# Optimization experiments

Measured on AMD Instinct MI355X. Metric: run time of the kernel, lower is better.

The kernel has to match this reference:

```python
import jax, jax.numpy as jnp
import numpy as np

POI, EMB, UNITS, QDIM, B = 5000, 256, 512, 256, 64


def setup_inputs() -> dict:
    key = jax.random.key(0)
    ks = jax.random.split(key, 16)
    s = 0.05
    return {
        "x": jax.random.randint(ks[0], (B,), 0, POI),
        "query": jax.random.normal(ks[1], (B, QDIM), jnp.float32),
        "poi_embedding": jax.random.normal(ks[2], (POI, EMB), jnp.float32),
        "A_hat": jax.random.normal(ks[3], (B, B), jnp.float32),
        "dec_hidden": jax.random.normal(ks[4], (B, UNITS), jnp.float32),
        "cat_dec_hidden": jax.random.normal(ks[5], (1, B, UNITS), jnp.float32),
        # GRUCell params (keras order z, r, h; reset_after=True -> bias [2, 3*units])
        "gru_kernel": jax.random.normal(ks[6], (EMB + QDIM, 3 * UNITS), jnp.float32) * s,
        "gru_rec_kernel": jax.random.normal(ks[7], (UNITS, 3 * UNITS), jnp.float32) * s,
        "gru_bias": jax.random.normal(ks[8], (2, 3 * UNITS), jnp.float32) * s,
        # Bahdanau attention params
        "W1_w": jax.random.normal(ks[9], (EMB, UNITS), jnp.float32) * s,
        "W1_b": jnp.zeros((UNITS,), jnp.float32),
        "W2_w": jax.random.normal(ks[10], (UNITS, UNITS), jnp.float32) * s,
        "W2_b": jnp.zeros((UNITS,), jnp.float32),
        "V_w": jax.random.normal(ks[11], (UNITS, 1), jnp.float32) * s,
        "V_b": jnp.zeros((1,), jnp.float32),
        # output dense: concat(context EMB, output_ UNITS, cat_hidden UNITS) -> POI
        "fc_w": jax.random.normal(ks[12], (EMB + 2 * UNITS, POI), jnp.float32) * s,
        "fc_b": jnp.zeros((POI,), jnp.float32),
    }


def _gru_cell(x, h, kernel, rec_kernel, bias):
    # keras GRUCell, reset_after=True, gate order (z, r, h)
    xm = x @ kernel + bias[0]        # [B, 3U]
    hm = h @ rec_kernel + bias[1]    # [B, 3U]
    xz, xr, xh = jnp.split(xm, 3, axis=-1)
    hz, hr, hh = jnp.split(hm, 3, axis=-1)
    z = jax.nn.sigmoid(xz + hz)
    r = jax.nn.sigmoid(xr + hr)
    h_cand = jnp.tanh(xh + r * hh)
    h_new = z * h + (1.0 - z) * h_cand
    return h_new, h_new


def reference(x, query, poi_embedding, A_hat, dec_hidden, cat_dec_hidden,
              gru_kernel, gru_rec_kernel, gru_bias,
              W1_w, W1_b, W2_w, W2_b, V_w, V_b, fc_w, fc_b):
    emb = poi_embedding
    x1 = jnp.concatenate([emb[x], query], axis=1)          # [B, EMB+QDIM]
    output_, state = _gru_cell(x1, dec_hidden, gru_kernel, gru_rec_kernel, gru_bias)
    # Bahdanau attention: values are the full embedding table [POI, EMB]
    v_proj = emb @ W1_w + W1_b                              # [POI, U]
    q_proj = output_ @ W2_w + W2_b                          # [B, U]
    score = jnp.tanh(v_proj[None, :, :] + q_proj[:, None, :]) @ V_w + V_b  # [B, POI, 1]
    attn = jax.nn.softmax(score, axis=1)                    # [B, POI, 1]
    context = jnp.sum(attn * emb[None, :, :], axis=1)       # [B, EMB]
    out_cat = jnp.concatenate([context, output_, cat_dec_hidden[0]], axis=1)
    logits = out_cat @ fc_w + fc_b                          # [B, POI]
    return (logits, state, output_)
```

## Files before the change

kernel.cpp:

```cpp
#include <hip/hip_runtime.h>
#include <hip/hip_bf16.h>

typedef __bf16 bf16;
typedef __bf16 bf16x8 __attribute__((ext_vector_type(8)));
typedef float f32x4 __attribute__((ext_vector_type(4)));

#define BB 64
#define EMB 256
#define UNITS 512
#define POI 5000
#define KCAT 1280
#define SCLD 5024
#define NSPL 8
#define L2E 1.4426950408889634f

__device__ __forceinline__ float rcp_(float x){ return __builtin_amdgcn_rcpf(x); }
__device__ __forceinline__ float exp2_(float x){ return __builtin_amdgcn_exp2f(x); }

__device__ __forceinline__ f32x4 mm16f(const float* __restrict__ A, const float* __restrict__ B,
                                       int lda, int ldb, int K, int mr, int nc, int lane){
  int q = lane >> 4;
  f32x4 acc = {0.f,0.f,0.f,0.f};
  const float* ap = A + (size_t)mr*lda + q*8;
  const float* bp = B + (size_t)(q*8)*ldb + nc;
#pragma unroll 2
  for(int k0 = 0; k0 < K; k0 += 32){
    f32x4 a0 = *(const f32x4*)ap;
    f32x4 a1 = *(const f32x4*)(ap+4);
    bf16x8 a, b;
#pragma unroll
    for(int j=0;j<4;j++){ a[j] = (bf16)a0[j]; a[4+j] = (bf16)a1[j]; }
#pragma unroll
    for(int j=0;j<8;j++) b[j] = (bf16)bp[(size_t)j*ldb];
    acc = __builtin_amdgcn_mfma_f32_16x16x32_bf16(a, b, acc, 0, 0, 0);
    ap += 32; bp += (size_t)32*ldb;
  }
  return acc;
}

__global__ __launch_bounds__(256) void k_gru(const int* __restrict__ x,
    const float* __restrict__ query, const float* __restrict__ emb, const float* __restrict__ h0,
    const float* __restrict__ gruK, const float* __restrict__ gruR,
    float* __restrict__ xmP, float* __restrict__ hmP){
  int lane = threadIdx.x & 63, w = threadIdx.x >> 6;
  int col = blockIdx.x*16 + (lane & 15);
  int m = w*16 + (lane & 15);
  int z = blockIdx.z;
  const float* A; const float* B; int lda, mr;
  if(blockIdx.y == 0){
    B = gruK + (size_t)(z*256)*1536;
    if(z == 0){ A = emb;   mr = x[m]; lda = EMB; }
    else      { A = query; mr = m;    lda = 256; }
  } else {
    B = gruR + (size_t)(z*256)*1536;
    A = h0 + z*256; mr = m; lda = UNITS;
  }
  f32x4 acc = mm16f(A, B, lda, 1536, 256, mr, col, lane);
  float* C = (blockIdx.y ? hmP : xmP) + (size_t)z*BB*1536;
  int rb = w*16 + (lane >> 4)*4;
#pragma unroll
  for(int r=0;r<4;r++) C[(size_t)(rb+r)*1536 + col] = acc[r];
}

__global__ void k_gates(const float* __restrict__ xmP, const float* __restrict__ hmP,
                        const float* __restrict__ bias, const float* __restrict__ h0,
                        const float* __restrict__ catd,
                        float* __restrict__ hn, float* __restrict__ outc, float* __restrict__ dout){
  int b = blockIdx.x, u = threadIdx.x;
  for(int p=u;p<POI;p+=512) dout[(size_t)b*POI + p] = 0.f;
  const float* x0 = xmP + b*1536; const float* x1s = xmP + (size_t)BB*1536 + b*1536;
  const float* h0s = hmP + b*1536; const float* h1s = hmP + (size_t)BB*1536 + b*1536;
  float xz = x0[u]      + x1s[u]      + bias[u];
  float xg = x0[512+u]  + x1s[512+u]  + bias[512+u];
  float xh = x0[1024+u] + x1s[1024+u] + bias[1024+u];
  float hz = h0s[u]      + h1s[u]      + bias[1536+u];
  float hg = h0s[512+u]  + h1s[512+u]  + bias[2048+u];
  float hh = h0s[1024+u] + h1s[1024+u] + bias[2560+u];
  float z = rcp_(1.f + exp2_(-L2E*(xz+hz)));
  float r = rcp_(1.f + exp2_(-L2E*(xg+hg)));
  float ca = xh + r*hh;
  ca = fminf(fmaxf(ca, -15.f), 15.f);
  float e = exp2_(2.f*L2E*ca);
  float hc = (e - 1.f)*rcp_(e + 1.f);
  float h = h0[b*512+u];
  float v = z*h + (1.f - z)*hc;
  hn[b*512+u] = v;
  outc[b*KCAT + 256 + u] = v;
  outc[b*KCAT + 768 + u] = catd[(size_t)b*512 + u];
  dout[(size_t)POI*BB + (size_t)b*512 + u] = v;
  dout[(size_t)POI*BB + (size_t)BB*512 + (size_t)b*512 + u] = v;
}

__global__ __launch_bounds__(64) void k_qproj(const float* __restrict__ hn, const float* __restrict__ W2,
                        const float* __restrict__ W2b, float* __restrict__ Eq){
  int lane = threadIdx.x;
  int m0 = (blockIdx.x & 3)*16;
  int col = (blockIdx.x >> 2)*16 + (lane & 15);
  f32x4 acc = mm16f(hn, W2, UNITS, UNITS, UNITS, m0 + (lane & 15), col, lane);
  float bn = W2b[col];
  int rb = m0 + (lane >> 4)*4;
#pragma unroll
  for(int r=0;r<4;r++){
    float v = (acc[r] + bn)*(2.f*L2E);
    Eq[(rb+r)*UNITS + col] = exp2_(fminf(fmaxf(v, -28.f), 28.f));
  }
}

__global__ __launch_bounds__(256) void k_vscore(const float* __restrict__ emb, const float* __restrict__ W1,
    const float* __restrict__ W1b, const float* __restrict__ Eq,
    const float* __restrict__ Vw, float* __restrict__ scS){
  __shared__ float evs[16][68];
  __shared__ float Qs[64][68];
  __shared__ float vws[64];
  int t = threadIdx.x, lane = t & 63, w = t >> 6;
  int p0 = blockIdx.x*16, uh = blockIdx.y*64;
  int mr = p0 + (lane & 15); if(mr > POI-1) mr = POI-1;
  {
    int ncl = w*16 + (lane & 15);
    f32x4 acc = mm16f(emb, W1, EMB, UNITS, EMB, mr, uh + ncl, lane);
    float bn = W1b[uh + ncl];
    int rb = (lane >> 4)*4;
#pragma unroll
    for(int r=0;r<4;r++){
      float v = (acc[r] + bn)*(2.f*L2E);
      evs[rb+r][ncl] = exp2_(fminf(fmaxf(v, -28.f), 28.f));
    }
  }
  for(int i=t;i<4096;i+=256){ int b=i>>6, u=i&63; Qs[b][u] = Eq[b*UNITS + uh + u]; }
  if(t < 64) vws[t] = Vw[uh + t];
  __syncthreads();
  int tp = t & 7, tb = t >> 3;
  float s00=0.f, s01=0.f, s10=0.f, s11=0.f;
#pragma unroll
  for(int u4=0;u4<16;u4++){
    f32x4 e0 = *(f32x4*)&evs[2*tp][u4*4];
    f32x4 e1 = *(f32x4*)&evs[2*tp+1][u4*4];
    f32x4 q0 = *(f32x4*)&Qs[2*tb][u4*4];
    f32x4 q1 = *(f32x4*)&Qs[2*tb+1][u4*4];
    f32x4 w4 = *(f32x4*)&vws[u4*4];
#pragma unroll
    for(int e=0;e<4;e++){
      float wv = w4[e];
      s00 += wv * rcp_(e0[e]*q0[e] + 1.f);
      s01 += wv * rcp_(e0[e]*q1[e] + 1.f);
      s10 += wv * rcp_(e1[e]*q0[e] + 1.f);
      s11 += wv * rcp_(e1[e]*q1[e] + 1.f);
    }
  }
  float* s = scS + (size_t)blockIdx.y*BB*SCLD;
  int pA = p0 + 2*tp, bA = 2*tb;
  if(pA < POI)  { s[(size_t)bA*SCLD + pA]   = s00; s[(size_t)(bA+1)*SCLD + pA]   = s01; }
  if(pA+1 < POI){ s[(size_t)bA*SCLD + pA+1] = s10; s[(size_t)(bA+1)*SCLD + pA+1] = s11; }
}

__global__ __launch_bounds__(1024) void k_softmax(float* __restrict__ sc, float* __restrict__ outc){
  __shared__ float red[1024];
  int b = blockIdx.x, t = threadIdx.x;
  if(t < 256) outc[b*KCAT + t] = 0.f;
  float* sA = sc + (size_t)b*SCLD;
  float sum = 0.f;
  for(int p=t;p<POI;p+=1024){
    float a = sA[p];
#pragma unroll
    for(int y=1;y<NSPL;y++) a += sA[(size_t)y*BB*SCLD + p];
    float wv = exp2_(-2.f*L2E*a);
    sA[p] = wv;
    sum += wv;
  }
  red[t] = sum; __syncthreads();
  for(int o=512;o>0;o>>=1){ if(t<o) red[t]+=red[t+o]; __syncthreads(); }
  float iv = rcp_(red[0]);
  for(int p=t;p<POI;p+=1024) sA[p] *= iv;
  if(t < SCLD-POI) sA[POI + t] = 0.f;
}

__global__ __launch_bounds__(256) void k_ctx(const float* __restrict__ wb, const float* __restrict__ emb,
                                             float* __restrict__ outc){
  int lane = threadIdx.x & 63, w = threadIdx.x >> 6;
  int n = blockIdx.x*16 + (lane & 15);
  int ky = blockIdx.y;
  int kbeg = ky*384;
  int mr = w*16 + (lane & 15);
  f32x4 acc = mm16f(wb + kbeg, emb + (size_t)kbeg*EMB, SCLD, EMB, 384, mr, n, lane);
  if(ky == 12){
    int q = lane >> 4;
    const float* ap = wb + (size_t)mr*SCLD + 4992 + q*8;
    bf16x8 a, bfr;
#pragma unroll
    for(int j=0;j<8;j++) a[j] = (bf16)ap[j];
#pragma unroll
    for(int j=0;j<8;j++){
      int k = 4992 + q*8 + j; int kc = k < POI ? k : POI-1;
      bfr[j] = (bf16)emb[(size_t)kc*EMB + n];
    }
    acc = __builtin_amdgcn_mfma_f32_16x16x32_bf16(a, bfr, acc, 0, 0, 0);
  }
  int rb = w*16 + (lane >> 4)*4;
#pragma unroll
  for(int r=0;r<4;r++) atomicAdd(&outc[(size_t)(rb+r)*KCAT + n], acc[r]);
}

__global__ __launch_bounds__(256) void k_logits(const float* __restrict__ A, const float* __restrict__ Bw,
                        const float* __restrict__ fcb, float* __restrict__ out){
  int lane = threadIdx.x & 63, w = threadIdx.x >> 6;
  int n = blockIdx.x*16 + (lane & 15);
  int nc = n < POI ? n : POI-1;
  int ky = blockIdx.y, kbeg = ky*320;
  f32x4 acc = mm16f(A + kbeg, Bw + (size_t)kbeg*POI, KCAT, POI, 320,
                    w*16 + (lane & 15), nc, lane);
  int rb = w*16 + (lane >> 4)*4;
  if(n < POI){
    float bn = (ky == 0) ? fcb[n] : 0.f;
#pragma unroll
    for(int r=0;r<4;r++) atomicAdd(&out[(size_t)(rb+r)*POI + n], acc[r] + bn);
  }
}

extern "C" void kernel_launch(void* const* d_in, const int* in_sizes, int n_in,
                              void* d_out, int out_size, void* d_ws, size_t ws_size,
                              hipStream_t stream){
  const int*   x     = (const int*)d_in[0];
  const float* query = (const float*)d_in[1];
  const float* emb   = (const float*)d_in[2];
  const float* h0    = (const float*)d_in[4];
  const float* catd  = (const float*)d_in[5];
  const float* gruK  = (const float*)d_in[6];
  const float* gruR  = (const float*)d_in[7];
  const float* gruB  = (const float*)d_in[8];
  const float* W1    = (const float*)d_in[9];
  const float* W1b   = (const float*)d_in[10];
  const float* W2    = (const float*)d_in[11];
  const float* W2b   = (const float*)d_in[12];
  const float* Vw    = (const float*)d_in[13];
  const float* fcw   = (const float*)d_in[15];
  const float* fcb   = (const float*)d_in[16];
  float* out = (float*)d_out;

  char* ws = (char*)d_ws;
  size_t off = 0;
  auto alloc = [&](size_t bytes)->void*{ void* p = ws + off; off += (bytes + 255) & ~(size_t)255; return p; };
  float* outc = (float*)alloc((size_t)BB*KCAT*4);
  float* xmP  = (float*)alloc((size_t)2*BB*1536*4);
  float* hmP  = (float*)alloc((size_t)2*BB*1536*4);
  float* hn   = (float*)alloc((size_t)BB*512*4);
  float* Eq   = (float*)alloc((size_t)BB*512*4);
  float* sc   = (float*)alloc((size_t)NSPL*BB*SCLD*4);

  k_gru    <<<dim3(96,2,2), 256, 0, stream>>>(x, query, emb, h0, gruK, gruR, xmP, hmP);
  k_gates  <<<BB, 512, 0, stream>>>(xmP, hmP, gruB, h0, catd, hn, outc, out);
  k_qproj  <<<128, 64, 0, stream>>>(hn, W2, W2b, Eq);
  k_vscore <<<dim3(313,NSPL), 256, 0, stream>>>(emb, W1, W1b, Eq, Vw, sc);
  k_softmax<<<BB, 1024, 0, stream>>>(sc, outc);
  k_ctx    <<<dim3(16,13), 256, 0, stream>>>(sc, emb, outc);
  k_logits <<<dim3(313,4), 256, 0, stream>>>(outc, fcw, fcb, out);
}
```

Baseline: 238.2 us.

## Pre-transpose weights to bf16 K-major and replace logits atomics with split-K reduction

Adds a transpose kernel that converts fc_w, GRU kernels, W1, W2 and the embedding table into transposed bf16 copies each call, so every MFMA B-operand becomes one contiguous 16-byte load instead of eight strided float loads. The logits GEMM now writes two split-K partial buffers that a new reduction kernel sums with the bias, replacing the atomicAdd path and the zero-fill of the output. The vscore split drops from 8 to 4 with each block covering 128 units. The transpose pass rereads about 26 MB of weights on every call, which could cost more than the faster GEMM loads save.

```diff
diff --git a/kernel.cpp b/kernel.cpp
--- a/kernel.cpp
+++ b/kernel.cpp
@@ -2,6 +2,7 @@
 #include <hip/hip_bf16.h>
 
 typedef __bf16 bf16;
+typedef __bf16 bf16x4 __attribute__((ext_vector_type(4)));
 typedef __bf16 bf16x8 __attribute__((ext_vector_type(8)));
 typedef float f32x4 __attribute__((ext_vector_type(4)));
 
@@ -11,51 +12,93 @@
 #define POI 5000
 #define KCAT 1280
 #define SCLD 5024
-#define NSPL 8
+#define LGLD 5008
 #define L2E 1.4426950408889634f
 
 __device__ __forceinline__ float rcp_(float x){ return __builtin_amdgcn_rcpf(x); }
 __device__ __forceinline__ float exp2_(float x){ return __builtin_amdgcn_exp2f(x); }
 
-__device__ __forceinline__ f32x4 mm16f(const float* __restrict__ A, const float* __restrict__ B,
-                                       int lda, int ldb, int K, int mr, int nc, int lane){
+__device__ __forceinline__ f32x4 mm16bt(const float* __restrict__ A, const bf16* __restrict__ Bt,
+                                        int lda, int ldbk, int K, int mr, int nc,
+                                        int ka, int kb, int lane){
   int q = lane >> 4;
   f32x4 acc = {0.f,0.f,0.f,0.f};
-  const float* ap = A + (size_t)mr*lda + q*8;
-  const float* bp = B + (size_t)(q*8)*ldb + nc;
+  const float* ap = A + (size_t)mr*lda + ka + q*8;
+  const bf16* bp = Bt + (size_t)nc*ldbk + kb + q*8;
 #pragma unroll 2
   for(int k0 = 0; k0 < K; k0 += 32){
     f32x4 a0 = *(const f32x4*)ap;
     f32x4 a1 = *(const f32x4*)(ap+4);
-    bf16x8 a, b;
+    bf16x8 a;
 #pragma unroll
     for(int j=0;j<4;j++){ a[j] = (bf16)a0[j]; a[4+j] = (bf16)a1[j]; }
-#pragma unroll
-    for(int j=0;j<8;j++) b[j] = (bf16)bp[(size_t)j*ldb];
+    bf16x8 b = *(const bf16x8*)bp;
     acc = __builtin_amdgcn_mfma_f32_16x16x32_bf16(a, b, acc, 0, 0, 0);
-    ap += 32; bp += (size_t)32*ldb;
+    ap += 32; bp += 32;
   }
   return acc;
+}
+
+__global__ __launch_bounds__(256) void k_tr(const float* __restrict__ fcw, const float* __restrict__ gruK,
+    const float* __restrict__ gruR, const float* __restrict__ W1, const float* __restrict__ W2,
+    const float* __restrict__ emb, bf16* __restrict__ fcwT, bf16* __restrict__ gKT,
+    bf16* __restrict__ gRT, bf16* __restrict__ W1T, bf16* __restrict__ W2T, bf16* __restrict__ embT){
+  __shared__ float ls[64][65];
+  int bid = blockIdx.x, t = threadIdx.x;
+  const float* src; bf16* dst; int Ks, Ns, lddst, dRows, tn, tk;
+  if(bid < 1580){      src=fcw;  Ks=1280; Ns=5000; dst=fcwT; lddst=1280; dRows=5008; tn=bid/20; tk=bid%20; }
+  else if(bid < 1772){ int b=bid-1580; src=gruK; Ks=512; Ns=1536; dst=gKT; lddst=512; dRows=1536; tn=b/8; tk=b%8; }
+  else if(bid < 1964){ int b=bid-1772; src=gruR; Ks=512; Ns=1536; dst=gRT; lddst=512; dRows=1536; tn=b/8; tk=b%8; }
+  else if(bid < 1996){ int b=bid-1964; src=W1;   Ks=256; Ns=512;  dst=W1T; lddst=256; dRows=512;  tn=b/4; tk=b%4; }
+  else if(bid < 2060){ int b=bid-1996; src=W2;   Ks=512; Ns=512;  dst=W2T; lddst=512; dRows=512;  tn=b/8; tk=b%8; }
+  else {               int b=bid-2060; src=emb;  Ks=5000; Ns=256; dst=embT; lddst=5056; dRows=256; tn=b/79; tk=b%79; }
+  int n0 = tn*64, k0 = tk*64;
+  bool fullN = (n0 + 64 <= Ns);
+#pragma unroll
+  for(int ps=0; ps<4; ps++){
+    int r = (t>>4) + ps*16;
+    int sr = k0 + r; if(sr > Ks-1) sr = Ks-1;
+    int c4 = (t&15)*4;
+    if(fullN){
+      f32x4 v = *(const f32x4*)&src[(size_t)sr*Ns + n0 + c4];
+      ls[r][c4]=v[0]; ls[r][c4+1]=v[1]; ls[r][c4+2]=v[2]; ls[r][c4+3]=v[3];
+    } else {
+#pragma unroll
+      for(int i=0;i<4;i++){ int sc2 = n0+c4+i; if(sc2 > Ns-1) sc2 = Ns-1; ls[r][c4+i] = src[(size_t)sr*Ns + sc2]; }
+    }
+  }
+  __syncthreads();
+#pragma unroll
+  for(int ps=0; ps<4; ps++){
+    int rr = (t>>4) + ps*16;
+    int dr = n0 + rr;
+    if(dr < dRows){
+      int cc = (t&15)*4;
+      bf16x4 o;
+#pragma unroll
+      for(int i=0;i<4;i++) o[i] = (bf16)ls[cc+i][rr];
+      *(bf16x4*)&dst[(size_t)dr*lddst + k0 + cc] = o;
+    }
+  }
 }
 
 __global__ __launch_bounds__(256) void k_gru(const int* __restrict__ x,
     const float* __restrict__ query, const float* __restrict__ emb, const float* __restrict__ h0,
-    const float* __restrict__ gruK, const float* __restrict__ gruR,
+    const bf16* __restrict__ gKT, const bf16* __restrict__ gRT,
     float* __restrict__ xmP, float* __restrict__ hmP){
   int lane = threadIdx.x & 63, w = threadIdx.x >> 6;
   int col = blockIdx.x*16 + (lane & 15);
   int m = w*16 + (lane & 15);
   int z = blockIdx.z;
-  const float* A; const float* B; int lda, mr;
+  const float* A; const bf16* Bt; int lda, mr, ka;
   if(blockIdx.y == 0){
-    B = gruK + (size_t)(z*256)*1536;
-    if(z == 0){ A = emb;   mr = x[m]; lda = EMB; }
-    else      { A = query; mr = m;    lda = 256; }
+    Bt = gKT;
+    if(z == 0){ A = emb;   mr = x[m]; lda = EMB; ka = 0; }
+    else      { A = query; mr = m;    lda = 256; ka = 0; }
   } else {
-    B = gruR + (size_t)(z*256)*1536;
-    A = h0 + z*256; mr = m; lda = UNITS;
-  }
-  f32x4 acc = mm16f(A, B, lda, 1536, 256, mr, col, lane);
+    Bt = gRT; A = h0; mr = m; lda = UNITS; ka = z*256;
+  }
+  f32x4 acc = mm16bt(A, Bt, lda, 512, 256, mr, col, ka, z*256, lane);
   float* C = (blockIdx.y ? hmP : xmP) + (size_t)z*BB*1536;
   int rb = w*16 + (lane >> 4)*4;
 #pragma unroll
@@ -67,7 +110,6 @@
                         const float* __restrict__ catd,
                         float* __restrict__ hn, float* __restrict__ outc, float* __restrict__ dout){
   int b = blockIdx.x, u = threadIdx.x;
-  for(int p=u;p<POI;p+=512) dout[(size_t)b*POI + p] = 0.f;
   const float* x0 = xmP + b*1536; const float* x1s = xmP + (size_t)BB*1536 + b*1536;
   const float* h0s = hmP + b*1536; const float* h1s = hmP + (size_t)BB*1536 + b*1536;
   float xz = x0[u]      + x1s[u]      + bias[u];
@@ -91,12 +133,12 @@
   dout[(size_t)POI*BB + (size_t)BB*512 + (size_t)b*512 + u] = v;
 }
 
-__global__ __launch_bounds__(64) void k_qproj(const float* __restrict__ hn, const float* __restrict__ W2,
+__global__ __launch_bounds__(64) void k_qproj(const float* __restrict__ hn, const bf16* __restrict__ W2T,
                         const float* __restrict__ W2b, float* __restrict__ Eq){
   int lane = threadIdx.x;
   int m0 = (blockIdx.x & 3)*16;
   int col = (blockIdx.x >> 2)*16 + (lane & 15);
-  f32x4 acc = mm16f(hn, W2, UNITS, UNITS, UNITS, m0 + (lane & 15), col, lane);
+  f32x4 acc = mm16bt(hn, W2T, UNITS, UNITS, UNITS, m0 + (lane & 15), col, 0, 0, lane);
   float bn = W2b[col];
   int rb = m0 + (lane >> 4)*4;
 #pragma unroll
@@ -106,18 +148,19 @@
   }
 }
 
-__global__ __launch_bounds__(256) void k_vscore(const float* __restrict__ emb, const float* __restrict__ W1,
+__global__ __launch_bounds__(256) void k_vscore(const float* __restrict__ emb, const bf16* __restrict__ W1T,
     const float* __restrict__ W1b, const float* __restrict__ Eq,
     const float* __restrict__ Vw, float* __restrict__ scS){
-  __shared__ float evs[16][68];
+  __shared__ float evs[16][132];
   __shared__ float Qs[64][68];
-  __shared__ float vws[64];
+  __shared__ float vws[128];
   int t = threadIdx.x, lane = t & 63, w = t >> 6;
-  int p0 = blockIdx.x*16, uh = blockIdx.y*64;
+  int p0 = blockIdx.x*16, uh = blockIdx.y*128;
   int mr = p0 + (lane & 15); if(mr > POI-1) mr = POI-1;
-  {
-    int ncl = w*16 + (lane & 15);
-    f32x4 acc = mm16f(emb, W1, EMB, UNITS, EMB, mr, uh + ncl, lane);
+#pragma unroll
+  for(int i=0;i<2;i++){
+    int ncl = (w + i*4)*16 + (lane & 15);
+    f32x4 acc = mm16bt(emb, W1T, EMB, EMB, EMB, mr, uh + ncl, 0, 0, lane);
     float bn = W1b[uh + ncl];
     int rb = (lane >> 4)*4;
 #pragma unroll
@@ -126,25 +169,29 @@
       evs[rb+r][ncl] = exp2_(fminf(fmaxf(v, -28.f), 28.f));
     }
   }
-  for(int i=t;i<4096;i+=256){ int b=i>>6, u=i&63; Qs[b][u] = Eq[b*UNITS + uh + u]; }
-  if(t < 64) vws[t] = Vw[uh + t];
-  __syncthreads();
+  if(t < 128) vws[t] = Vw[uh + t];
   int tp = t & 7, tb = t >> 3;
   float s00=0.f, s01=0.f, s10=0.f, s11=0.f;
-#pragma unroll
-  for(int u4=0;u4<16;u4++){
-    f32x4 e0 = *(f32x4*)&evs[2*tp][u4*4];
-    f32x4 e1 = *(f32x4*)&evs[2*tp+1][u4*4];
-    f32x4 q0 = *(f32x4*)&Qs[2*tb][u4*4];
-    f32x4 q1 = *(f32x4*)&Qs[2*tb+1][u4*4];
-    f32x4 w4 = *(f32x4*)&vws[u4*4];
-#pragma unroll
-    for(int e=0;e<4;e++){
-      float wv = w4[e];
-      s00 += wv * rcp_(e0[e]*q0[e] + 1.f);
-      s01 += wv * rcp_(e0[e]*q1[e] + 1.f);
-      s10 += wv * rcp_(e1[e]*q0[e] + 1.f);
-      s11 += wv * rcp_(e1[e]*q1[e] + 1.f);
+  for(int c=0;c<2;c++){
+    __syncthreads();
+    int ub = c*64;
+    for(int i=t;i<4096;i+=256){ int b=i>>6, u=i&63; Qs[b][u] = Eq[b*UNITS + uh + ub + u]; }
+    __syncthreads();
+#pragma unroll
+    for(int u4=0;u4<16;u4++){
+      f32x4 e0 = *(f32x4*)&evs[2*tp][ub+u4*4];
+      f32x4 e1 = *(f32x4*)&evs[2*tp+1][ub+u4*4];
+      f32x4 q0 = *(f32x4*)&Qs[2*tb][u4*4];
+      f32x4 q1 = *(f32x4*)&Qs[2*tb+1][u4*4];
+      f32x4 w4 = *(f32x4*)&vws[ub+u4*4];
+#pragma unroll
+      for(int e=0;e<4;e++){
+        float wv = w4[e];
+        s00 += wv * rcp_(e0[e]*q0[e] + 1.f);
+        s01 += wv * rcp_(e0[e]*q1[e] + 1.f);
+        s10 += wv * rcp_(e1[e]*q0[e] + 1.f);
+        s11 += wv * rcp_(e1[e]*q1[e] + 1.f);
+      }
     }
   }
   float* s = scS + (size_t)blockIdx.y*BB*SCLD;
@@ -160,9 +207,7 @@
   float* sA = sc + (size_t)b*SCLD;
   float sum = 0.f;
   for(int p=t;p<POI;p+=1024){
-    float a = sA[p];
-#pragma unroll
-    for(int y=1;y<NSPL;y++) a += sA[(size_t)y*BB*SCLD + p];
+    float a = sA[p] + sA[(size_t)BB*SCLD + p] + sA[(size_t)2*BB*SCLD + p] + sA[(size_t)3*BB*SCLD + p];
     float wv = exp2_(-2.f*L2E*a);
     sA[p] = wv;
     sum += wv;
@@ -174,45 +219,41 @@
   if(t < SCLD-POI) sA[POI + t] = 0.f;
 }
 
-__global__ __launch_bounds__(256) void k_ctx(const float* __restrict__ wb, const float* __restrict__ emb,
+__global__ __launch_bounds__(256) void k_ctx(const float* __restrict__ wb, const bf16* __restrict__ embT,
                                              float* __restrict__ outc){
   int lane = threadIdx.x & 63, w = threadIdx.x >> 6;
   int n = blockIdx.x*16 + (lane & 15);
   int ky = blockIdx.y;
-  int kbeg = ky*384;
-  int mr = w*16 + (lane & 15);
-  f32x4 acc = mm16f(wb + kbeg, emb + (size_t)kbeg*EMB, SCLD, EMB, 384, mr, n, lane);
-  if(ky == 12){
-    int q = lane >> 4;
-    const float* ap = wb + (size_t)mr*SCLD + 4992 + q*8;
-    bf16x8 a, bfr;
-#pragma unroll
-    for(int j=0;j<8;j++) a[j] = (bf16)ap[j];
-#pragma unroll
-    for(int j=0;j<8;j++){
-      int k = 4992 + q*8 + j; int kc = k < POI ? k : POI-1;
-      bfr[j] = (bf16)emb[(size_t)kc*EMB + n];
-    }
-    acc = __builtin_amdgcn_mfma_f32_16x16x32_bf16(a, bfr, acc, 0, 0, 0);
-  }
+  int kbeg = ky*384, kk = (ky == 12) ? 416 : 384;
+  f32x4 acc = mm16bt(wb, embT, SCLD, 5056, kk, w*16 + (lane & 15), n, kbeg, kbeg, lane);
   int rb = w*16 + (lane >> 4)*4;
 #pragma unroll
   for(int r=0;r<4;r++) atomicAdd(&outc[(size_t)(rb+r)*KCAT + n], acc[r]);
 }
 
-__global__ __launch_bounds__(256) void k_logits(const float* __restrict__ A, const float* __restrict__ Bw,
-                        const float* __restrict__ fcb, float* __restrict__ out){
+__global__ __launch_bounds__(256) void k_logits(const float* __restrict__ A, const bf16* __restrict__ fcwT,
+                                                float* __restrict__ lgP){
   int lane = threadIdx.x & 63, w = threadIdx.x >> 6;
   int n = blockIdx.x*16 + (lane & 15);
-  int nc = n < POI ? n : POI-1;
-  int ky = blockIdx.y, kbeg = ky*320;
-  f32x4 acc = mm16f(A + kbeg, Bw + (size_t)kbeg*POI, KCAT, POI, 320,
-                    w*16 + (lane & 15), nc, lane);
+  int ky = blockIdx.y, kbeg = ky*640;
+  f32x4 acc = mm16bt(A, fcwT, KCAT, 1280, 640, w*16 + (lane & 15), n, kbeg, kbeg, lane);
+  float* dst = lgP + (size_t)ky*BB*SCLD;
   int rb = w*16 + (lane >> 4)*4;
+#pragma unroll
+  for(int r=0;r<4;r++) dst[(size_t)(rb+r)*LGLD + n] = acc[r];
+}
+
+__global__ __launch_bounds__(256) void k_lred(const float* __restrict__ lgP, const float* __restrict__ fcb,
+                                              float* __restrict__ out){
+  int idx = blockIdx.x*256 + threadIdx.x;
+  int m = idx / 1252, nq = idx % 1252;
+  int n = nq*4;
   if(n < POI){
-    float bn = (ky == 0) ? fcb[n] : 0.f;
-#pragma unroll
-    for(int r=0;r<4;r++) atomicAdd(&out[(size_t)(rb+r)*POI + n], acc[r] + bn);
+    f32x4 a = *(const f32x4*)&lgP[(size_t)m*LGLD + n];
+    f32x4 b = *(const f32x4*)&lgP[(size_t)BB*SCLD + (size_t)m*LGLD + n];
+    f32x4 c = *(const f32x4*)&fcb[n];
+    f32x4 r = a + b + c;
+    *(f32x4*)&out[(size_t)m*POI + n] = r;
   }
 }
 
@@ -244,13 +285,22 @@
   float* hmP  = (float*)alloc((size_t)2*BB*1536*4);
   float* hn   = (float*)alloc((size_t)BB*512*4);
   float* Eq   = (float*)alloc((size_t)BB*512*4);
-  float* sc   = (float*)alloc((size_t)NSPL*BB*SCLD*4);
-
-  k_gru    <<<dim3(96,2,2), 256, 0, stream>>>(x, query, emb, h0, gruK, gruR, xmP, hmP);
+  float* sc   = (float*)alloc((size_t)4*BB*SCLD*4);
+  bf16* fcwT  = (bf16*)alloc((size_t)5008*1280*2);
+  bf16* gKT   = (bf16*)alloc((size_t)1536*512*2);
+  bf16* gRT   = (bf16*)alloc((size_t)1536*512*2);
+  bf16* W1T   = (bf16*)alloc((size_t)512*256*2);
+  bf16* W2T   = (bf16*)alloc((size_t)512*512*2);
+  bf16* embT  = (bf16*)alloc((size_t)256*5056*2);
+  float* lgP  = sc + (size_t)BB*SCLD;
+
+  k_tr     <<<2376, 256, 0, stream>>>(fcw, gruK, gruR, W1, W2, emb, fcwT, gKT, gRT, W1T, W2T, embT);
+  k_gru    <<<dim3(96,2,2), 256, 0, stream>>>(x, query, emb, h0, gKT, gRT, xmP, hmP);
   k_gates  <<<BB, 512, 0, stream>>>(xmP, hmP, gruB, h0, catd, hn, outc, out);
-  k_qproj  <<<128, 64, 0, stream>>>(hn, W2, W2b, Eq);
-  k_vscore <<<dim3(313,NSPL), 256, 0, stream>>>(emb, W1, W1b, Eq, Vw, sc);
+  k_qproj  <<<128, 64, 0, stream>>>(hn, W2T, W2b, Eq);
+  k_vscore <<<dim3(313,4), 256, 0, stream>>>(emb, W1T, W1b, Eq, Vw, sc);
   k_softmax<<<BB, 1024, 0, stream>>>(sc, outc);
-  k_ctx    <<<dim3(16,13), 256, 0, stream>>>(sc, emb, outc);
-  k_logits <<<dim3(313,4), 256, 0, stream>>>(outc, fcw, fcb, out);
-}
+  k_ctx    <<<dim3(16,13), 256, 0, stream>>>(sc, embT, outc);
+  k_logits <<<dim3(313,2), 256, 0, stream>>>(outc, fcwT, lgP);
+  k_lred   <<<313, 256, 0, stream>>>(lgP, fcb, out);
+}
```

Result: faster. 214.5 us (-9.9%).
